# Optimization experiments

Hardware: AMD Instinct MI355X
Metric: run time of the kernel (lower is better)

The kernel has to match this reference:

```python
import jax, jax.numpy as jnp
import numpy as np

D = 384        # residual_depth
QK = 48        # D // qk_dim_div(=8)
E = 768        # D * expand_factor(=2)
NB = 8         # num_blocks
VOCAB = 100
LN_EPS = 1e-5


def _ln(x, g, b):
    m = x.mean(-1, keepdims=True)
    v = x.var(-1, keepdims=True)  # biased, matches torch LayerNorm
    return (x - m) / jnp.sqrt(v + LN_EPS) * g + b


def setup_inputs() -> dict:
    key = jax.random.key(0)
    ks = jax.random.split(key, 5)
    B, S = 4, 2048
    q = jax.random.randint(ks[0], (B, S), 0, 100, dtype=jnp.int32)
    freqs = jnp.exp(jnp.arange(0, D, 2, dtype=jnp.float32) * (-np.log(10000.0) / D))
    # fused expand: rows = qk + qk + expand + expand = 1632
    exp_w = (0.5 / np.sqrt(D) / 2.0) * jax.random.normal(ks[1], (NB, 2 * QK + 2 * E, D), dtype=jnp.float32)
    proj_w = (1.0 / np.sqrt(D) / 2.0 / NB) * jax.random.normal(ks[2], (NB, D, E), dtype=jnp.float32)
    blk_g = jnp.ones((NB, D), jnp.float32)
    blk_b = jnp.zeros((NB, D), jnp.float32)
    ln_g = jnp.ones((D,), jnp.float32)
    ln_b = jnp.zeros((D,), jnp.float32)
    out_w = 0.02 * jax.random.normal(ks[3], (VOCAB, D), dtype=jnp.float32)
    return dict(q=q, freqs=freqs, exp_w=exp_w, proj_w=proj_w,
                blk_g=blk_g, blk_b=blk_b, ln_g=ln_g, ln_b=ln_b, out_w=out_w)


def reference(q, freqs, exp_w, proj_w, blk_g, blk_b, ln_g, ln_b, out_w):
    S = q.shape[1]
    # sinusoidal encoding of integer tokens -> [B,S,D]
    qe = q.astype(jnp.float32)[..., None] * freqs
    x = jnp.concatenate([jnp.sin(qe), jnp.cos(qe)], axis=-1)
    x = _ln(x, ln_g, ln_b)
    # causal mask; position_bias_base is zeros in the source
    bias = jnp.where(jnp.tril(jnp.ones((S, S), bool)), 0.0, -jnp.inf).astype(jnp.float32)
    inv_sqrt_qk = 1.0 / np.sqrt(QK)

    def block(x, p):
        ew, pw, g, b = p
        xn = _ln(x, g, b)
        h = xn @ ew.T                                   # [B,S,1632]
        qh, kh, lin, pg = jnp.split(h, [QK, 2 * QK, 2 * QK + E], axis=-1)
        geglu = lin * jax.nn.gelu(pg, approximate=False)  # [B,S,E]
        loc, val = geglu[..., :E - D], geglu[..., E - D:]  # [B,S,D],[B,S,D]
        sc = jnp.einsum('bqd,bkd->bqk', qh, kh) * inv_sqrt_qk + bias
        attn = jax.nn.softmax(sc, axis=-1) @ val          # [B,S,D]
        out = jnp.concatenate([loc, attn], axis=-1) @ pw.T
        return x + out, None

    x, _ = jax.lax.scan(block, x, (exp_w, proj_w, blk_g, blk_b))
    x = _ln(x, ln_g, ln_b)
    return x @ out_w.T
```

## Files before the change

### kernel.cpp

```cpp
#include <hip/hip_runtime.h>
#include <hip/hip_bf16.h>

#define TOK 8192
#define DM 384
#define QKD 48
#define EM 768
#define NBLK 8
#define NVOCAB 100
#define SEQ 2048
#define HN 1664
#define HNV 1632
#define CH 8
#define NUNITS 2304

using short4v = __attribute__((ext_vector_type(4))) short;
using short8 = __attribute__((ext_vector_type(8))) short;
using f32x4  = __attribute__((ext_vector_type(4))) float;

static __device__ __forceinline__ float bf2f(short s) {
    union { unsigned u; float f; } c; c.u = ((unsigned)(unsigned short)s) << 16; return c.f;
}
static __device__ __forceinline__ short f2bf(float f) {
    union { float f; unsigned u; } c; c.f = f;
    unsigned r = (c.u + 0x7FFFu + ((c.u >> 16) & 1u)) >> 16;
    return (short)r;
}
static __device__ __forceinline__ void gload_lds16(const short* g, short* l) {
    __builtin_amdgcn_global_load_lds((const __attribute__((address_space(1))) void*)g,
                                     (__attribute__((address_space(3))) void*)l, 16, 0, 0);
}

__global__ __launch_bounds__(256) void k_setup(const float* __restrict__ expw,
        const float* __restrict__ projw, const float* __restrict__ outw,
        short* __restrict__ ewb, short* __restrict__ pwb, short* __restrict__ owb,
        const int* __restrict__ q, const float* __restrict__ freqs,
        const float* __restrict__ lng, const float* __restrict__ lnb,
        const float* __restrict__ bg0, const float* __restrict__ bb0,
        float* __restrict__ x, short* __restrict__ xn) {
    const int n1 = NBLK * HN * DM;
    for (int i = blockIdx.x * 256 + threadIdx.x; i < n1; i += gridDim.x * 256) {
        int L = i / (HN * DM); int rem = i % (HN * DM);
        int r = rem / DM; int c = rem % DM;
        float v = (r < HNV) ? expw[((size_t)L * HNV + r) * DM + c] : 0.f;
        ewb[i] = f2bf(v);
    }
    const int n2 = NBLK * DM * EM;
    for (int i = blockIdx.x * 256 + threadIdx.x; i < n2; i += gridDim.x * 256)
        pwb[i] = f2bf(projw[i]);
    const int n3 = 128 * DM;
    for (int i = blockIdx.x * 256 + threadIdx.x; i < n3; i += gridDim.x * 256) {
        int r = i / DM, c = i % DM;
        owb[i] = f2bf(r < NVOCAB ? outw[r * DM + c] : 0.f);
    }
    int wid = blockIdx.x * 4 + (threadIdx.x >> 6);
    int lane = threadIdx.x & 63;
    float qv = (float)q[wid];
    float v[6]; float s = 0.f, s2 = 0.f;
    #pragma unroll
    for (int i = 0; i < 6; ++i) {
        int d = lane + 64 * i;
        float val;
        if (d < 192) val = sinf(qv * freqs[d]);
        else         val = cosf(qv * freqs[d - 192]);
        v[i] = val; s += val; s2 += val * val;
    }
    #pragma unroll
    for (int m = 1; m < 64; m <<= 1) { s += __shfl_xor(s, m); s2 += __shfl_xor(s2, m); }
    float mean = s * (1.f / DM);
    float var = s2 * (1.f / DM) - mean * mean;
    float rstd = rsqrtf(var + 1e-5f);
    float* xr = x + (size_t)wid * DM;
    float s3 = 0.f, s4 = 0.f;
    #pragma unroll
    for (int i = 0; i < 6; ++i) {
        int d = lane + 64 * i;
        v[i] = (v[i] - mean) * rstd * lng[d] + lnb[d];
        xr[d] = v[i];
        s3 += v[i]; s4 += v[i] * v[i];
    }
    #pragma unroll
    for (int m = 1; m < 64; m <<= 1) { s3 += __shfl_xor(s3, m); s4 += __shfl_xor(s4, m); }
    float mean2 = s3 * (1.f / DM);
    float var2 = s4 * (1.f / DM) - mean2 * mean2;
    float rstd2 = rsqrtf(var2 + 1e-5f);
    short* xo = xn + (size_t)wid * DM;
    #pragma unroll
    for (int i = 0; i < 6; ++i) {
        int d = lane + 64 * i;
        xo[d] = f2bf((v[i] - mean2) * rstd2 * bg0[d] + bb0[d]);
    }
}

__global__ __launch_bounds__(256) void k_ln(const float* __restrict__ x,
        const float* __restrict__ g, const float* __restrict__ b,
        short* __restrict__ xn) {
    int wid = blockIdx.x * 4 + (threadIdx.x >> 6);
    int lane = threadIdx.x & 63;
    if (wid >= TOK) return;
    const float* xr = x + (size_t)wid * DM;
    float v[6]; float s = 0.f, s2 = 0.f;
    #pragma unroll
    for (int i = 0; i < 6; ++i) {
        v[i] = xr[lane + 64 * i]; s += v[i]; s2 += v[i] * v[i];
    }
    #pragma unroll
    for (int m = 1; m < 64; m <<= 1) { s += __shfl_xor(s, m); s2 += __shfl_xor(s2, m); }
    float mean = s * (1.f / DM);
    float var = s2 * (1.f / DM) - mean * mean;
    float rstd = rsqrtf(var + 1e-5f);
    short* xo = xn + (size_t)wid * DM;
    #pragma unroll
    for (int i = 0; i < 6; ++i) {
        int d = lane + 64 * i;
        xo[d] = f2bf((v[i] - mean) * rstd * g[d] + b[d]);
    }
}

__global__ __launch_bounds__(256) void k_gemmh(const short* __restrict__ A,
        const short* __restrict__ Bw, short* __restrict__ cat,
        short* __restrict__ vT, short* __restrict__ qhb, short* __restrict__ khb) {
    __shared__ __align__(16) short As[128 * 64];
    __shared__ __align__(16) short Bs[128 * 64];
    int m0 = blockIdx.x * 128;
    int y = blockIdx.y;
    int t = threadIdx.x;
    int wid = t >> 6, lane = t & 63;
    int wm = (wid >> 1) * 64, wn = (wid & 1) * 64;
    int lr = lane & 15, lg = lane >> 4;
    int srow = wid * 32 + (lane >> 3);
    int sck = (lane & 7) ^ (lane >> 3);
    auto bmap = [&](int row) {
        if (y < 12) {
            int sh = row >> 4;
            return 96 + (sh & 1) * 768 + y * 64 + (sh >> 1) * 16 + (row & 15);
        }
        return (row < 96) ? row : 1632 + (row - 96);
    };
    const short* srcA[4]; const short* srcB[4]; short* dstA[4]; short* dstB[4];
    #pragma unroll
    for (int i = 0; i < 4; ++i) {
        int row = srow + i * 8;
        srcA[i] = A + (size_t)(m0 + row) * DM + sck * 8;
        srcB[i] = Bw + (size_t)bmap(row) * DM + sck * 8;
        dstA[i] = As + wid * 2048 + i * 512;
        dstB[i] = Bs + wid * 2048 + i * 512;
    }
    const f32x4 vz = {0.f, 0.f, 0.f, 0.f};
    f32x4 acc[4][4];
    #pragma unroll
    for (int i = 0; i < 4; ++i)
        #pragma unroll
        for (int j = 0; j < 4; ++j) acc[i][j] = vz;
    for (int k0 = 0; k0 < DM; k0 += 64) {
        if (k0) __syncthreads();
        #pragma unroll
        for (int i = 0; i < 4; ++i) {
            gload_lds16(srcA[i] + k0, dstA[i]);
            gload_lds16(srcB[i] + k0, dstB[i]);
        }
        __syncthreads();
        #pragma unroll
        for (int ks = 0; ks < 2; ++ks) {
            short8 af[4], bfr[4];
            #pragma unroll
            for (int i = 0; i < 4; ++i) {
                int ra = wm + i * 16 + lr;
                int rb = wn + i * 16 + lr;
                af[i]  = *(const short8*)(As + ra * 64 + (((lg + ks * 4) ^ (ra & 7)) * 8));
                bfr[i] = *(const short8*)(Bs + rb * 64 + (((lg + ks * 4) ^ (rb & 7)) * 8));
            }
            #pragma unroll
            for (int i = 0; i < 4; ++i)
                #pragma unroll
                for (int j = 0; j < 4; ++j)
                    acc[i][j] = __builtin_amdgcn_mfma_f32_16x16x32_bf16(af[i], bfr[j], acc[i][j], 0, 0, 0);
        }
    }
    if (y < 12) {
        #pragma unroll
        for (int i = 0; i < 4; ++i) {
            int tok0 = m0 + wm + i * 16 + lg * 4;
            #pragma unroll
            for (int k = 0; k < 2; ++k) {
                int e = y * 64 + (wn >> 1) + k * 16 + lr;
                short vb[4];
                #pragma unroll
                for (int r = 0; r < 4; ++r) {
                    float l = acc[i][2 * k][r], pg = acc[i][2 * k + 1][r];
                    float gel = pg * 0.5f * (1.f + erff(pg * 0.70710678118654752f));
                    vb[r] = f2bf(l * gel);
                }
                if (y < 6) {
                    #pragma unroll
                    for (int r = 0; r < 4; ++r)
                        cat[(size_t)(tok0 + r) * EM + e] = vb[r];
                } else {
                    short4v pk = {vb[0], vb[1], vb[2], vb[3]};
                    *(short4v*)(vT + (size_t)(e - DM) * TOK + tok0) = pk;
                }
            }
        }
    } else {
        #pragma unroll
        for (int i = 0; i < 4; ++i)
            #pragma unroll
            for (int j = 0; j < 4; ++j) {
                int col = wn + j * 16 + lr;
                #pragma unroll
                for (int r = 0; r < 4; ++r) {
                    int tok = m0 + wm + i * 16 + lg * 4 + r;
                    short v = f2bf(acc[i][j][r]);
                    if (col < 64) qhb[(size_t)tok * 64 + col] = (col < QKD) ? v : (short)0;
                    if (col >= QKD && col < QKD + 64)
                        khb[(size_t)tok * 64 + col - QKD] = (col < 96) ? v : (short)0;
                }
            }
    }
}

template<int MODE>
__global__ __launch_bounds__(256) void k_gemm(const short* __restrict__ A,
        const short* __restrict__ Bw, int K, int lda, int ldb,
        void* __restrict__ Cp, int ldc) {
    __shared__ __align__(16) short As[128 * 32];
    __shared__ __align__(16) short Bs[128 * 32];
    int m0 = blockIdx.x * 128, n0 = blockIdx.y * 128;
    int t = threadIdx.x;
    int wid = t >> 6, lane = t & 63;
    int wm = (wid >> 1) * 64, wn = (wid & 1) * 64;
    int lr = lane & 15, lg = lane >> 4;
    int seg0 = wid * 2, seg1 = wid * 2 + 1;
    int row0 = seg0 * 16 + (lane >> 2), row1 = seg1 * 16 + (lane >> 2);
    int cu0 = (lane & 3) ^ ((row0 + (row0 >> 2)) & 3);
    int cu1 = (lane & 3) ^ ((row1 + (row1 >> 2)) & 3);
    const short* srcA0 = A + (size_t)(m0 + row0) * lda + cu0 * 8;
    const short* srcA1 = A + (size_t)(m0 + row1) * lda + cu1 * 8;
    const short* srcB0 = Bw + (size_t)(n0 + row0) * ldb + cu0 * 8;
    const short* srcB1 = Bw + (size_t)(n0 + row1) * ldb + cu1 * 8;
    short* dA0 = As + seg0 * 512; short* dA1 = As + seg1 * 512;
    short* dB0 = Bs + seg0 * 512; short* dB1 = Bs + seg1 * 512;
    const f32x4 vz = {0.f, 0.f, 0.f, 0.f};
    f32x4 acc[4][4];
    #pragma unroll
    for (int i = 0; i < 4; ++i)
        #pragma unroll
        for (int j = 0; j < 4; ++j) acc[i][j] = vz;
    for (int k0 = 0; k0 < K; k0 += 32) {
        if (k0) __syncthreads();
        gload_lds16(srcA0 + k0, dA0);
        gload_lds16(srcA1 + k0, dA1);
        gload_lds16(srcB0 + k0, dB0);
        gload_lds16(srcB1 + k0, dB1);
        __syncthreads();
        short8 af[4], bfr[4];
        #pragma unroll
        for (int i = 0; i < 4; ++i) {
            int ra = wm + i * 16 + lr;
            int rb = wn + i * 16 + lr;
            af[i]  = *(const short8*)(As + ra * 32 + ((lg ^ ((ra + (ra >> 2)) & 3)) * 8));
            bfr[i] = *(const short8*)(Bs + rb * 32 + ((lg ^ ((rb + (rb >> 2)) & 3)) * 8));
        }
        #pragma unroll
        for (int i = 0; i < 4; ++i)
            #pragma unroll
            for (int j = 0; j < 4; ++j)
                acc[i][j] = __builtin_amdgcn_mfma_f32_16x16x32_bf16(af[i], bfr[j], acc[i][j], 0, 0, 0);
    }
    int rb = m0 + wm + (lane >> 4) * 4;
    int cb = n0 + wn + lr;
    #pragma unroll
    for (int i = 0; i < 4; ++i)
        #pragma unroll
        for (int j = 0; j < 4; ++j)
            #pragma unroll
            for (int r = 0; r < 4; ++r) {
                int row = rb + i * 16 + r;
                int col = cb + j * 16;
                float v = acc[i][j][r];
                if (MODE == 0) ((short*)Cp)[(size_t)row * ldc + col] = f2bf(v);
                else if (MODE == 1) ((float*)Cp)[(size_t)row * ldc + col] += v;
                else if (col < NVOCAB) ((float*)Cp)[(size_t)row * NVOCAB + col] = v;
            }
}

__global__ __launch_bounds__(128) void k_gemm64(const short* __restrict__ A,
        const short* __restrict__ Bw, float* __restrict__ C) {
    __shared__ __align__(16) short As[64 * 32];
    __shared__ __align__(16) short Bs[128 * 32];
    int m0 = blockIdx.x * 64, n0 = blockIdx.y * 128;
    int t = threadIdx.x;
    int wid = t >> 6, lane = t & 63;
    int wn = wid * 64;
    int lr = lane & 15, lg = lane >> 4;
    int rsub = lane >> 2;
    int rowA0 = (wid * 2) * 16 + rsub,     rowA1 = (wid * 2 + 1) * 16 + rsub;
    int rowB0 = (wid * 4) * 16 + rsub,     rowB1 = (wid * 4 + 1) * 16 + rsub;
    int rowB2 = (wid * 4 + 2) * 16 + rsub, rowB3 = (wid * 4 + 3) * 16 + rsub;
    int q4 = lane & 3;
    int cA0 = q4 ^ ((rowA0 + (rowA0 >> 2)) & 3), cA1 = q4 ^ ((rowA1 + (rowA1 >> 2)) & 3);
    int cB0 = q4 ^ ((rowB0 + (rowB0 >> 2)) & 3), cB1 = q4 ^ ((rowB1 + (rowB1 >> 2)) & 3);
    int cB2 = q4 ^ ((rowB2 + (rowB2 >> 2)) & 3), cB3 = q4 ^ ((rowB3 + (rowB3 >> 2)) & 3);
    const short* sA0 = A + (size_t)(m0 + rowA0) * EM + cA0 * 8;
    const short* sA1 = A + (size_t)(m0 + rowA1) * EM + cA1 * 8;
    const short* sB0 = Bw + (size_t)(n0 + rowB0) * EM + cB0 * 8;
    const short* sB1 = Bw + (size_t)(n0 + rowB1) * EM + cB1 * 8;
    const short* sB2 = Bw + (size_t)(n0 + rowB2) * EM + cB2 * 8;
    const short* sB3 = Bw + (size_t)(n0 + rowB3) * EM + cB3 * 8;
    short* dA0 = As + (wid * 2) * 512;     short* dA1 = As + (wid * 2 + 1) * 512;
    short* dB0 = Bs + (wid * 4) * 512;     short* dB1 = Bs + (wid * 4 + 1) * 512;
    short* dB2 = Bs + (wid * 4 + 2) * 512; short* dB3 = Bs + (wid * 4 + 3) * 512;
    const f32x4 vz = {0.f, 0.f, 0.f, 0.f};
    f32x4 acc[4][4];
    #pragma unroll
    for (int i = 0; i < 4; ++i)
        #pragma unroll
        for (int j = 0; j < 4; ++j) acc[i][j] = vz;
    for (int k0 = 0; k0 < EM; k0 += 32) {
        if (k0) __syncthreads();
        gload_lds16(sA0 + k0, dA0);
        gload_lds16(sA1 + k0, dA1);
        gload_lds16(sB0 + k0, dB0);
        gload_lds16(sB1 + k0, dB1);
        gload_lds16(sB2 + k0, dB2);
        gload_lds16(sB3 + k0, dB3);
        __syncthreads();
        short8 af[4], bfr[4];
        #pragma unroll
        for (int i = 0; i < 4; ++i) {
            int ra = i * 16 + lr;
            int rbw = wn + i * 16 + lr;
            af[i]  = *(const short8*)(As + ra * 32 + ((lg ^ ((ra + (ra >> 2)) & 3)) * 8));
            bfr[i] = *(const short8*)(Bs + rbw * 32 + ((lg ^ ((rbw + (rbw >> 2)) & 3)) * 8));
        }
        #pragma unroll
        for (int i = 0; i < 4; ++i)
            #pragma unroll
            for (int j = 0; j < 4; ++j)
                acc[i][j] = __builtin_amdgcn_mfma_f32_16x16x32_bf16(af[i], bfr[j], acc[i][j], 0, 0, 0);
    }
    int rbase = m0 + (lane >> 4) * 4;
    int cbase = n0 + wn + lr;
    #pragma unroll
    for (int i = 0; i < 4; ++i)
        #pragma unroll
        for (int j = 0; j < 4; ++j)
            #pragma unroll
            for (int r = 0; r < 4; ++r)
                C[(size_t)(rbase + i * 16 + r) * DM + cbase + j * 16] += acc[i][j][r];
}

__global__ __launch_bounds__(256) void k_flash(const short* __restrict__ qhb,
        const short* __restrict__ khb, const short* __restrict__ vT,
        short* __restrict__ Po, float* __restrict__ Pml) {
    int idx = blockIdx.x;
    int xcd = idx & 7;
    int b = xcd >> 1;
    int unit = ((idx >> 3) << 1) | (xcd & 1);
    int gq = unit & 31, c = unit >> 5;
    if (c > (gq >> 2)) return;
    __shared__ __align__(16) short Vlds[384 * 40];
    __shared__ __align__(16) short Klds[32 * 64];
    __shared__ __align__(16) short Plds[4 * 16 * 40];
    int t = threadIdx.x;
    int wid = t >> 6, lane = t & 63;
    int lr = lane & 15, lg = lane >> 4;
    int qt = gq * 4 + wid;
    int g = qt >> 4;
    int tb = b * SEQ;
    int q0 = qt * 16;
    int nkbm = 2 * gq + 2;
    int kb0 = c * CH;
    int kb1 = min(kb0 + CH, nkbm);
    short* P = Plds + wid * (16 * 40);
    const float scale = 0.14433756729740643f;
    const float CFIX = 8.f;
    const f32x4 vzero = {0.f, 0.f, 0.f, 0.f};

    short8 qf[2];
    #pragma unroll
    for (int ks = 0; ks < 2; ++ks)
        qf[ks] = *(const short8*)(qhb + (size_t)(tb + q0 + lr) * 64 + ks * 32 + lg * 8);

    f32x4 o[24];
    #pragma unroll
    for (int j = 0; j < 24; ++j) o[j] = vzero;
    float li[4];
    #pragma unroll
    for (int r = 0; r < 4; ++r) li[r] = 0.f;

    int vrow = t >> 2, vc = (t & 3) * 8;
    const short* vsrc0 = vT + (size_t)vrow * TOK + tb + vc;
    int krow = t >> 3, kc8 = (t & 7) * 8;
    const short* ksrc0 = khb + (size_t)(tb + krow) * 64 + kc8;

    short8 rv[6], rk;
    #pragma unroll
    for (int i = 0; i < 6; ++i)
        rv[i] = *(const short8*)(vsrc0 + (size_t)(i * 64) * TOK + kb0 * 32);
    rk = *(const short8*)(ksrc0 + (size_t)kb0 * 2048);

    for (int kb = kb0; kb < kb1; ++kb) {
        int kbase = kb * 32;
        __syncthreads();
        #pragma unroll
        for (int i = 0; i < 6; ++i)
            *(short8*)(Vlds + (vrow + i * 64) * 40 + vc) = rv[i];
        *(short8*)(Klds + krow * 64 + kc8) = rk;
        if (kb + 1 < kb1) {
            #pragma unroll
            for (int i = 0; i < 6; ++i)
                rv[i] = *(const short8*)(vsrc0 + (size_t)(i * 64) * TOK + kbase + 32);
            rk = *(const short8*)(ksrc0 + (size_t)(kb + 1) * 2048);
        }
        __syncthreads();
        short8 kf0a = *(const short8*)(Klds + lr * 64 + lg * 8);
        short8 kf0b = *(const short8*)(Klds + lr * 64 + 32 + lg * 8);
        short8 kf1a = *(const short8*)(Klds + (16 + lr) * 64 + lg * 8);
        short8 kf1b = *(const short8*)(Klds + (16 + lr) * 64 + 32 + lg * 8);

        f32x4 s0 = vzero, s1 = vzero;
        s0 = __builtin_amdgcn_mfma_f32_16x16x32_bf16(qf[0], kf0a, s0, 0, 0, 0);
        s0 = __builtin_amdgcn_mfma_f32_16x16x32_bf16(qf[1], kf0b, s0, 0, 0, 0);
        s1 = __builtin_amdgcn_mfma_f32_16x16x32_bf16(qf[0], kf1a, s1, 0, 0, 0);
        s1 = __builtin_amdgcn_mfma_f32_16x16x32_bf16(qf[1], kf1b, s1, 0, 0, 0);

        bool needmask = (kbase + 31 > q0);
        #pragma unroll
        for (int r = 0; r < 4; ++r) {
            float v0 = s0[r] * scale, v1 = s1[r] * scale;
            if (needmask) {
                int qg = q0 + lg * 4 + r;
                if (kbase + lr > qg) v0 = -1e30f;
                if (kbase + 16 + lr > qg) v1 = -1e30f;
            }
            float p0 = __expf(v0 - CFIX);
            float p1 = __expf(v1 - CFIX);
            li[r] += p0 + p1;
            s0[r] = p0; s1[r] = p1;
        }
        #pragma unroll
        for (int r = 0; r < 4; ++r) {
            P[(lg * 4 + r) * 40 + lr] = f2bf(s0[r]);
            P[(lg * 4 + r) * 40 + 16 + lr] = f2bf(s1[r]);
        }
        short8 pf = *(const short8*)(P + lr * 40 + lg * 8);
        #pragma unroll
        for (int j = 0; j < 24; ++j) {
            short8 vf = *(const short8*)(Vlds + (j * 16 + lr) * 40 + lg * 8);
            o[j] = __builtin_amdgcn_mfma_f32_16x16x32_bf16(pf, vf, o[j], 0, 0, 0);
        }
    }
    #pragma unroll
    for (int r = 0; r < 4; ++r) {
        float sum = li[r];
        #pragma unroll
        for (int d2 = 1; d2 < 16; d2 <<= 1) sum += __shfl_xor(sum, d2);
        li[r] = sum;
    }
    int uid = 8 * g * (g + 1) + (qt & 15) * (g + 1) + c;
    int sidx = (uid << 2) | b;
    size_t ob = (size_t)sidx * (16 * 384);
    #pragma unroll
    for (int j = 0; j < 24; ++j)
        #pragma unroll
        for (int r = 0; r < 4; ++r)
            Po[ob + (size_t)(lg * 4 + r) * 384 + j * 16 + lr] = f2bf(o[j][r]);
    if (lr == 0) {
        #pragma unroll
        for (int r = 0; r < 4; ++r)
            Pml[sidx * 32 + 16 + lg * 4 + r] = li[r];
    }
}

__global__ __launch_bounds__(256) void k_comb(const short* __restrict__ Po,
        const float* __restrict__ Pml, short* __restrict__ cat) {
    int bid = blockIdx.x;
    int b = bid & 3, qt = bid >> 2;
    int g = qt >> 4;
    int nch = g + 1;
    int ubase = 8 * g * (g + 1) + (qt & 15) * (g + 1);
    int tid = threadIdx.x;
    int row = tid >> 4;
    int c0 = (tid & 15) * 24;
    float L = 0.f;
    float acc[24];
    #pragma unroll
    for (int e = 0; e < 24; ++e) acc[e] = 0.f;
    #pragma unroll
    for (int c = 0; c < 8; ++c) {
        if (c < nch) {
            int uu = ((ubase + c) << 2) | b;
            L += Pml[uu * 32 + 16 + row];
            const short8* pp = (const short8*)(Po + ((size_t)uu * 16 + row) * 384 + c0);
            #pragma unroll
            for (int v = 0; v < 3; ++v) {
                short8 tv = pp[v];
                #pragma unroll
                for (int k = 0; k < 8; ++k) acc[v * 8 + k] += bf2f(tv[k]);
            }
        }
    }
    float invL = 1.f / L;
    size_t tok = (size_t)b * SEQ + qt * 16 + row;
    short* dst = cat + tok * EM + DM + c0;
    #pragma unroll
    for (int v = 0; v < 3; ++v) {
        short8 o8;
        #pragma unroll
        for (int k = 0; k < 8; ++k) o8[k] = f2bf(acc[v * 8 + k] * invL);
        *(short8*)(dst + v * 8) = o8;
    }
}

extern "C" void kernel_launch(void* const* d_in, const int* in_sizes, int n_in,
                              void* d_out, int out_size, void* d_ws, size_t ws_size,
                              hipStream_t stream) {
    const int*   q     = (const int*)d_in[0];
    const float* freqs = (const float*)d_in[1];
    const float* expw  = (const float*)d_in[2];
    const float* projw = (const float*)d_in[3];
    const float* blkg  = (const float*)d_in[4];
    const float* blkb  = (const float*)d_in[5];
    const float* lng   = (const float*)d_in[6];
    const float* lnb   = (const float*)d_in[7];
    const float* outw  = (const float*)d_in[8];
    float* out = (float*)d_out;

    char* p = (char*)d_ws;
    auto alloc = [&](size_t bytes) {
        char* r = p; p += (bytes + 255) & ~(size_t)255; return r;
    };
    float* x   = (float*)alloc((size_t)TOK * DM * 4);
    short* xn  = (short*)alloc((size_t)TOK * DM * 2);
    short* h   = (short*)alloc((size_t)TOK * HN * 2);
    short* cat = (short*)alloc((size_t)TOK * EM * 2);
    short* vT  = (short*)alloc((size_t)DM * TOK * 2);
    short* qhb = (short*)alloc((size_t)TOK * 64 * 2);
    short* khb = (short*)alloc((size_t)TOK * 64 * 2);
    short* ewb = (short*)alloc((size_t)NBLK * HN * DM * 2);
    short* pwb = (short*)alloc((size_t)NBLK * DM * EM * 2);
    short* owb = (short*)alloc((size_t)128 * DM * 2);
    (void)h;
    short* Po  = xn;
    float* Pml = (float*)(Po + (size_t)NUNITS * 16 * 384);

    k_setup<<<2048, 256, 0, stream>>>(expw, projw, outw, ewb, pwb, owb,
                                      q, freqs, lng, lnb, blkg, blkb, x, xn);

    for (int L = 0; L < NBLK; ++L) {
        if (L) k_ln<<<TOK / 4, 256, 0, stream>>>(x, blkg + L * DM, blkb + L * DM, xn);
        k_gemmh<<<dim3(64, 13), 256, 0, stream>>>(xn, ewb + (size_t)L * HN * DM,
                                                  cat, vT, qhb, khb);
        k_flash<<<1024, 256, 0, stream>>>(qhb, khb, vT, Po, Pml);
        k_comb<<<512, 256, 0, stream>>>(Po, Pml, cat);
        k_gemm64<<<dim3(128, 3), 128, 0, stream>>>(cat, pwb + (size_t)L * DM * EM, x);
    }
    k_ln<<<TOK / 4, 256, 0, stream>>>(x, lng, lnb, xn);
    k_gemm<2><<<dim3(64, 1), 256, 0, stream>>>(xn, owb, DM, DM, DM, out, NVOCAB);
}
```

Before: 804.2 us.

## Use 8-wave flash blocks sharing K/V tiles across more query tiles

The flash attention kernel now launches 512-thread blocks covering 8 query tiles each instead of 4, so every staged K/V chunk in LDS is reused by twice as many waves. Query groups are enumerated in reverse order so the heaviest causal groups start first, and the per-thread V staging shrinks from 6 to 3 loads. This lowers global/LDS load traffic per unit of work but halves the grid and adds barrier cost with more waves per block. The split-to-combine indexing (Po/Pml unit layout) must still match k_comb, which was not changed.

```diff
diff --git a/kernel.cpp b/kernel.cpp
--- a/kernel.cpp
+++ b/kernel.cpp
@@ -349,28 +349,29 @@
                 C[(size_t)(rbase + i * 16 + r) * DM + cbase + j * 16] += acc[i][j][r];
 }
 
-__global__ __launch_bounds__(256) void k_flash(const short* __restrict__ qhb,
+__global__ __launch_bounds__(512) void k_flash(const short* __restrict__ qhb,
         const short* __restrict__ khb, const short* __restrict__ vT,
         short* __restrict__ Po, float* __restrict__ Pml) {
     int idx = blockIdx.x;
     int xcd = idx & 7;
     int b = xcd >> 1;
     int unit = ((idx >> 3) << 1) | (xcd & 1);
-    int gq = unit & 31, c = unit >> 5;
-    if (c > (gq >> 2)) return;
+    int gq8 = 15 - (unit & 15);
+    int c = unit >> 4;
+    int nkbm = 4 * gq8 + 4;
+    int kb0 = c * CH;
+    if (kb0 >= nkbm) return;
+    int kb1 = min(kb0 + CH, nkbm);
     __shared__ __align__(16) short Vlds[384 * 40];
     __shared__ __align__(16) short Klds[32 * 64];
-    __shared__ __align__(16) short Plds[4 * 16 * 40];
+    __shared__ __align__(16) short Plds[8 * 16 * 40];
     int t = threadIdx.x;
     int wid = t >> 6, lane = t & 63;
     int lr = lane & 15, lg = lane >> 4;
-    int qt = gq * 4 + wid;
+    int qt = gq8 * 8 + wid;
     int g = qt >> 4;
     int tb = b * SEQ;
     int q0 = qt * 16;
-    int nkbm = 2 * gq + 2;
-    int kb0 = c * CH;
-    int kb1 = min(kb0 + CH, nkbm);
     short* P = Plds + wid * (16 * 40);
     const float scale = 0.14433756729740643f;
     const float CFIX = 8.f;
@@ -393,24 +394,24 @@
     int krow = t >> 3, kc8 = (t & 7) * 8;
     const short* ksrc0 = khb + (size_t)(tb + krow) * 64 + kc8;
 
-    short8 rv[6], rk;
-    #pragma unroll
-    for (int i = 0; i < 6; ++i)
-        rv[i] = *(const short8*)(vsrc0 + (size_t)(i * 64) * TOK + kb0 * 32);
-    rk = *(const short8*)(ksrc0 + (size_t)kb0 * 2048);
+    short8 rv0, rv1, rv2, rk;
+    rv0 = *(const short8*)(vsrc0 + (size_t)0 * TOK * 128 + kb0 * 32);
+    rv1 = *(const short8*)(vsrc0 + (size_t)128 * TOK + kb0 * 32);
+    rv2 = *(const short8*)(vsrc0 + (size_t)256 * TOK + kb0 * 32);
+    if (t < 256) rk = *(const short8*)(ksrc0 + (size_t)kb0 * 2048);
 
     for (int kb = kb0; kb < kb1; ++kb) {
         int kbase = kb * 32;
         __syncthreads();
-        #pragma unroll
-        for (int i = 0; i < 6; ++i)
-            *(short8*)(Vlds + (vrow + i * 64) * 40 + vc) = rv[i];
-        *(short8*)(Klds + krow * 64 + kc8) = rk;
+        *(short8*)(Vlds + vrow * 40 + vc) = rv0;
+        *(short8*)(Vlds + (vrow + 128) * 40 + vc) = rv1;
+        *(short8*)(Vlds + (vrow + 256) * 40 + vc) = rv2;
+        if (t < 256) *(short8*)(Klds + krow * 64 + kc8) = rk;
         if (kb + 1 < kb1) {
-            #pragma unroll
-            for (int i = 0; i < 6; ++i)
-                rv[i] = *(const short8*)(vsrc0 + (size_t)(i * 64) * TOK + kbase + 32);
-            rk = *(const short8*)(ksrc0 + (size_t)(kb + 1) * 2048);
+            rv0 = *(const short8*)(vsrc0 + kbase + 32);
+            rv1 = *(const short8*)(vsrc0 + (size_t)128 * TOK + kbase + 32);
+            rv2 = *(const short8*)(vsrc0 + (size_t)256 * TOK + kbase + 32);
+            if (t < 256) rk = *(const short8*)(ksrc0 + (size_t)(kb + 1) * 2048);
         }
         __syncthreads();
         short8 kf0a = *(const short8*)(Klds + lr * 64 + lg * 8);
@@ -551,7 +552,7 @@
         if (L) k_ln<<<TOK / 4, 256, 0, stream>>>(x, blkg + L * DM, blkb + L * DM, xn);
         k_gemmh<<<dim3(64, 13), 256, 0, stream>>>(xn, ewb + (size_t)L * HN * DM,
                                                   cat, vT, qhb, khb);
-        k_flash<<<1024, 256, 0, stream>>>(qhb, khb, vT, Po, Pml);
+        k_flash<<<512, 512, 0, stream>>>(qhb, khb, vT, Po, Pml);
         k_comb<<<512, 256, 0, stream>>>(Po, Pml, cat);
         k_gemm64<<<dim3(128, 3), 128, 0, stream>>>(cat, pwb + (size_t)L * DM * EM, x);
     }
```

Result: no change. 809.9 us (+0.7%).

## Fuse output projection, residual add and next LayerNorm into one kernel

Applied to the files above, without the earlier changes.

Replaces the projection GEMM plus separate LayerNorm kernel with a single kernel where each 256-thread block computes a full 32-row by 384-column tile. It adds the residual, reduces row mean and variance across waves through shared memory, and writes both the fp32 residual and the bf16 normalized input for the next block, or for the final LN. This removes one launch per layer and a full read of x. The cost is a grid of only 256 blocks, fewer than the old 384, and each block reloads the whole weight matrix, which may lower parallelism and raise weight traffic.

```diff
diff --git a/kernel.cpp b/kernel.cpp
--- a/kernel.cpp
+++ b/kernel.cpp
@@ -88,31 +88,6 @@
     for (int i = 0; i < 6; ++i) {
         int d = lane + 64 * i;
         xo[d] = f2bf((v[i] - mean2) * rstd2 * bg0[d] + bb0[d]);
-    }
-}
-
-__global__ __launch_bounds__(256) void k_ln(const float* __restrict__ x,
-        const float* __restrict__ g, const float* __restrict__ b,
-        short* __restrict__ xn) {
-    int wid = blockIdx.x * 4 + (threadIdx.x >> 6);
-    int lane = threadIdx.x & 63;
-    if (wid >= TOK) return;
-    const float* xr = x + (size_t)wid * DM;
-    float v[6]; float s = 0.f, s2 = 0.f;
-    #pragma unroll
-    for (int i = 0; i < 6; ++i) {
-        v[i] = xr[lane + 64 * i]; s += v[i]; s2 += v[i] * v[i];
-    }
-    #pragma unroll
-    for (int m = 1; m < 64; m <<= 1) { s += __shfl_xor(s, m); s2 += __shfl_xor(s2, m); }
-    float mean = s * (1.f / DM);
-    float var = s2 * (1.f / DM) - mean * mean;
-    float rstd = rsqrtf(var + 1e-5f);
-    short* xo = xn + (size_t)wid * DM;
-    #pragma unroll
-    for (int i = 0; i < 6; ++i) {
-        int d = lane + 64 * i;
-        xo[d] = f2bf((v[i] - mean) * rstd * g[d] + b[d]);
     }
 }
 
@@ -283,70 +258,112 @@
             }
 }
 
-__global__ __launch_bounds__(128) void k_gemm64(const short* __restrict__ A,
-        const short* __restrict__ Bw, float* __restrict__ C) {
-    __shared__ __align__(16) short As[64 * 32];
-    __shared__ __align__(16) short Bs[128 * 32];
-    int m0 = blockIdx.x * 64, n0 = blockIdx.y * 128;
+__global__ __launch_bounds__(256) void k_gemmproj(const short* __restrict__ A,
+        const short* __restrict__ Bw, float* __restrict__ x,
+        short* __restrict__ xn, const float* __restrict__ g,
+        const float* __restrict__ b) {
+    __shared__ __align__(16) short As[32 * 32];
+    __shared__ __align__(16) short Bs[384 * 32];
+    __shared__ float redS[4][32];
+    __shared__ float redQ[4][32];
+    int m0 = blockIdx.x * 32;
     int t = threadIdx.x;
     int wid = t >> 6, lane = t & 63;
-    int wn = wid * 64;
     int lr = lane & 15, lg = lane >> 4;
-    int rsub = lane >> 2;
-    int rowA0 = (wid * 2) * 16 + rsub,     rowA1 = (wid * 2 + 1) * 16 + rsub;
-    int rowB0 = (wid * 4) * 16 + rsub,     rowB1 = (wid * 4 + 1) * 16 + rsub;
-    int rowB2 = (wid * 4 + 2) * 16 + rsub, rowB3 = (wid * 4 + 3) * 16 + rsub;
-    int q4 = lane & 3;
-    int cA0 = q4 ^ ((rowA0 + (rowA0 >> 2)) & 3), cA1 = q4 ^ ((rowA1 + (rowA1 >> 2)) & 3);
-    int cB0 = q4 ^ ((rowB0 + (rowB0 >> 2)) & 3), cB1 = q4 ^ ((rowB1 + (rowB1 >> 2)) & 3);
-    int cB2 = q4 ^ ((rowB2 + (rowB2 >> 2)) & 3), cB3 = q4 ^ ((rowB3 + (rowB3 >> 2)) & 3);
-    const short* sA0 = A + (size_t)(m0 + rowA0) * EM + cA0 * 8;
-    const short* sA1 = A + (size_t)(m0 + rowA1) * EM + cA1 * 8;
-    const short* sB0 = Bw + (size_t)(n0 + rowB0) * EM + cB0 * 8;
-    const short* sB1 = Bw + (size_t)(n0 + rowB1) * EM + cB1 * 8;
-    const short* sB2 = Bw + (size_t)(n0 + rowB2) * EM + cB2 * 8;
-    const short* sB3 = Bw + (size_t)(n0 + rowB3) * EM + cB3 * 8;
-    short* dA0 = As + (wid * 2) * 512;     short* dA1 = As + (wid * 2 + 1) * 512;
-    short* dB0 = Bs + (wid * 4) * 512;     short* dB1 = Bs + (wid * 4 + 1) * 512;
-    short* dB2 = Bs + (wid * 4 + 2) * 512; short* dB3 = Bs + (wid * 4 + 3) * 512;
+    const short* src[7]; short* dst[7]; bool valid[7];
+    int rin = lane >> 2, cch = lane & 3;
+    #pragma unroll
+    for (int qd = 0; qd < 7; ++qd) {
+        int seg = wid * 7 + qd;
+        valid[qd] = (seg < 26);
+        int segc = valid[qd] ? seg : 25;
+        if (segc < 2) {
+            int row = segc * 16 + rin;
+            int cu = cch ^ ((row + (row >> 2)) & 3);
+            src[qd] = A + (size_t)(m0 + row) * EM + cu * 8;
+            dst[qd] = As + segc * 512;
+        } else {
+            int row = (segc - 2) * 16 + rin;
+            int cu = cch ^ ((row + (row >> 2)) & 3);
+            src[qd] = Bw + (size_t)row * EM + cu * 8;
+            dst[qd] = Bs + (segc - 2) * 512;
+        }
+    }
     const f32x4 vz = {0.f, 0.f, 0.f, 0.f};
-    f32x4 acc[4][4];
-    #pragma unroll
-    for (int i = 0; i < 4; ++i)
-        #pragma unroll
-        for (int j = 0; j < 4; ++j) acc[i][j] = vz;
+    f32x4 acc[2][6];
+    #pragma unroll
+    for (int i = 0; i < 2; ++i)
+        #pragma unroll
+        for (int j = 0; j < 6; ++j) acc[i][j] = vz;
     for (int k0 = 0; k0 < EM; k0 += 32) {
         if (k0) __syncthreads();
-        gload_lds16(sA0 + k0, dA0);
-        gload_lds16(sA1 + k0, dA1);
-        gload_lds16(sB0 + k0, dB0);
-        gload_lds16(sB1 + k0, dB1);
-        gload_lds16(sB2 + k0, dB2);
-        gload_lds16(sB3 + k0, dB3);
+        #pragma unroll
+        for (int qd = 0; qd < 7; ++qd)
+            if (valid[qd]) gload_lds16(src[qd] + k0, dst[qd]);
         __syncthreads();
-        short8 af[4], bfr[4];
-        #pragma unroll
-        for (int i = 0; i < 4; ++i) {
+        short8 af[2], bfr[6];
+        #pragma unroll
+        for (int i = 0; i < 2; ++i) {
             int ra = i * 16 + lr;
-            int rbw = wn + i * 16 + lr;
-            af[i]  = *(const short8*)(As + ra * 32 + ((lg ^ ((ra + (ra >> 2)) & 3)) * 8));
-            bfr[i] = *(const short8*)(Bs + rbw * 32 + ((lg ^ ((rbw + (rbw >> 2)) & 3)) * 8));
-        }
-        #pragma unroll
-        for (int i = 0; i < 4; ++i)
-            #pragma unroll
-            for (int j = 0; j < 4; ++j)
+            af[i] = *(const short8*)(As + ra * 32 + ((lg ^ ((ra + (ra >> 2)) & 3)) * 8));
+        }
+        #pragma unroll
+        for (int j = 0; j < 6; ++j) {
+            int rb = wid * 96 + j * 16 + lr;
+            bfr[j] = *(const short8*)(Bs + rb * 32 + ((lg ^ ((rb + (rb >> 2)) & 3)) * 8));
+        }
+        #pragma unroll
+        for (int i = 0; i < 2; ++i)
+            #pragma unroll
+            for (int j = 0; j < 6; ++j)
                 acc[i][j] = __builtin_amdgcn_mfma_f32_16x16x32_bf16(af[i], bfr[j], acc[i][j], 0, 0, 0);
     }
-    int rbase = m0 + (lane >> 4) * 4;
-    int cbase = n0 + wn + lr;
-    #pragma unroll
-    for (int i = 0; i < 4; ++i)
-        #pragma unroll
-        for (int j = 0; j < 4; ++j)
-            #pragma unroll
-            for (int r = 0; r < 4; ++r)
-                C[(size_t)(rbase + i * 16 + r) * DM + cbase + j * 16] += acc[i][j][r];
+    #pragma unroll
+    for (int i = 0; i < 2; ++i) {
+        float rs[4], rq[4];
+        #pragma unroll
+        for (int r = 0; r < 4; ++r) {
+            int row = m0 + i * 16 + lg * 4 + r;
+            float s = 0.f, q2 = 0.f;
+            #pragma unroll
+            for (int j = 0; j < 6; ++j) {
+                int col = wid * 96 + j * 16 + lr;
+                float yv = x[(size_t)row * DM + col] + acc[i][j][r];
+                acc[i][j][r] = yv;
+                s += yv; q2 += yv * yv;
+            }
+            #pragma unroll
+            for (int m = 1; m < 16; m <<= 1) { s += __shfl_xor(s, m); q2 += __shfl_xor(q2, m); }
+            rs[r] = s; rq[r] = q2;
+        }
+        if (lr == 0) {
+            #pragma unroll
+            for (int r = 0; r < 4; ++r) {
+                redS[wid][i * 16 + lg * 4 + r] = rs[r];
+                redQ[wid][i * 16 + lg * 4 + r] = rq[r];
+            }
+        }
+    }
+    __syncthreads();
+    #pragma unroll
+    for (int i = 0; i < 2; ++i)
+        #pragma unroll
+        for (int r = 0; r < 4; ++r) {
+            int lrow = i * 16 + lg * 4 + r;
+            float s = redS[0][lrow] + redS[1][lrow] + redS[2][lrow] + redS[3][lrow];
+            float q2 = redQ[0][lrow] + redQ[1][lrow] + redQ[2][lrow] + redQ[3][lrow];
+            float mean = s * (1.f / DM);
+            float var = q2 * (1.f / DM) - mean * mean;
+            float rstd = rsqrtf(var + 1e-5f);
+            int row = m0 + lrow;
+            #pragma unroll
+            for (int j = 0; j < 6; ++j) {
+                int col = wid * 96 + j * 16 + lr;
+                float yv = acc[i][j][r];
+                x[(size_t)row * DM + col] = yv;
+                xn[(size_t)row * DM + col] = f2bf((yv - mean) * rstd * g[col] + b[col]);
+            }
+        }
 }
 
 __global__ __launch_bounds__(256) void k_flash(const short* __restrict__ qhb,
@@ -548,13 +565,13 @@
                                       q, freqs, lng, lnb, blkg, blkb, x, xn);
 
     for (int L = 0; L < NBLK; ++L) {
-        if (L) k_ln<<<TOK / 4, 256, 0, stream>>>(x, blkg + L * DM, blkb + L * DM, xn);
         k_gemmh<<<dim3(64, 13), 256, 0, stream>>>(xn, ewb + (size_t)L * HN * DM,
                                                   cat, vT, qhb, khb);
         k_flash<<<1024, 256, 0, stream>>>(qhb, khb, vT, Po, Pml);
         k_comb<<<512, 256, 0, stream>>>(Po, Pml, cat);
-        k_gemm64<<<dim3(128, 3), 128, 0, stream>>>(cat, pwb + (size_t)L * DM * EM, x);
-    }
-    k_ln<<<TOK / 4, 256, 0, stream>>>(x, lng, lnb, xn);
+        const float* gn = (L < NBLK - 1) ? blkg + (L + 1) * DM : lng;
+        const float* bn = (L < NBLK - 1) ? blkb + (L + 1) * DM : lnb;
+        k_gemmproj<<<256, 256, 0, stream>>>(cat, pwb + (size_t)L * DM * EM, x, xn, gn, bn);
+    }
     k_gemm<2><<<dim3(64, 1), 256, 0, stream>>>(xn, owb, DM, DM, DM, out, NVOCAB);
 }
```

New measurement: 743.1 us. 1.08x faster.
